# Kernel tuning notes

Measured on AMD Instinct MI355X. Metric: run time of the kernel, lower is better.

## Reference

```python
import jax, jax.numpy as jnp
import numpy as np

GAMMA = 1.0
N, M, D = 8192, 8192, 256


def setup_inputs() -> dict:
    key = jax.random.key(0)
    kx, ky = jax.random.split(key)
    x = jax.random.normal(kx, (N, D), dtype=jnp.float32)
    y = jax.random.normal(ky, (M, D), dtype=jnp.float32)
    return {"x": x, "y": y}


def reference(x, y):
    # Pairwise squared distances without materializing the (n, m, d) diff
    x2 = jnp.sum(x * x, axis=-1)              # (n,)
    y2 = jnp.sum(y * y, axis=-1)              # (m,)
    xy = jnp.einsum('nd,md->nm', x, y)        # (n, m)
    dist_sq = x2[:, None] + y2[None, :] - 2.0 * xy
    # clamp tiny negative values from cancellation to preserve exp(-g*d2)<=1
    dist_sq = jnp.maximum(dist_sq, 0.0)
    return jnp.exp(-GAMMA * dist_sq)
```

## Files before the change

### kernel.cpp

```cpp
#include <hip/hip_runtime.h>
#include <hip/hip_bf16.h>

typedef __attribute__((ext_vector_type(4))) float f32x4;
typedef __attribute__((ext_vector_type(8))) short bf16x8;
typedef __attribute__((ext_vector_type(16))) float f32x16;
typedef long i64t;

#define MSZ 8192
#define D_DIM 256
#define BM 128
#define BN 128
#define NTILES 8

#define GLOAD_LDS(g, s) __builtin_amdgcn_global_load_lds( \
    (const __attribute__((address_space(1))) unsigned int*)(g), \
    (__attribute__((address_space(3))) unsigned int*)(s), 16, 0, 0)

__device__ __forceinline__ unsigned short f2bf(float f) {
  __hip_bfloat16 h = __float2bfloat16(f);
  unsigned short u; __builtin_memcpy(&u, &h, 2); return u;
}

__global__ __launch_bounds__(256)
void prep_fp8(const float* __restrict__ X, const float* __restrict__ Y,
              unsigned char* __restrict__ Xq, unsigned char* __restrict__ Yq,
              float* __restrict__ x2, float* __restrict__ y2) {
  int gw = (blockIdx.x * 256 + threadIdx.x) >> 6;
  int l = threadIdx.x & 63;
  int row = gw & (MSZ - 1);
  const float* src = (gw < MSZ ? X : Y) + (size_t)row * D_DIM + l * 4;
  f32x4 v = *(const f32x4*)src;
  float ss = v[0]*v[0] + v[1]*v[1] + v[2]*v[2] + v[3]*v[3];
  int p = __builtin_amdgcn_cvt_pk_fp8_f32(v[0], v[1], 0, false);
  p = __builtin_amdgcn_cvt_pk_fp8_f32(v[2], v[3], p, true);
  unsigned char* dst = (gw < MSZ ? Xq : Yq) + (size_t)row * D_DIM + l * 4;
  *(unsigned int*)dst = (unsigned int)p;
  #pragma unroll
  for (int m = 1; m < 64; m <<= 1) ss += __shfl_xor(ss, m);
  if (l == 0) (gw < MSZ ? x2 : y2)[row] = ss;
}

__global__ __launch_bounds__(256, 2)
void rbf_main(const unsigned char* __restrict__ Xq, const unsigned char* __restrict__ Yq,
              const float* __restrict__ X2, const float* __restrict__ Y2,
              float* __restrict__ Out) {
  __shared__ __align__(16) unsigned char Al[BM * D_DIM];
  __shared__ __align__(16) unsigned char Bl[BN * D_DIM];
  __shared__ float sx2[BM];

  int bid = blockIdx.x;
  int swz = (bid & 7) * 64 + (bid >> 3);
  int bm = swz >> 3;
  int rowBase = bm * BM;
  int colBase = ((swz & 7) << 3) * BN;

  int tid = threadIdx.x;
  int l = tid & 63;
  int w = tid >> 6;
  int wr = w >> 1, wc = w & 1;

  if (tid < BM) sx2[tid] = X2[rowBase + tid];

  #pragma unroll
  for (int q = 0; q < 8; ++q) {
    int c = tid + 256 * q;
    int row = c >> 4, g = c & 15;
    GLOAD_LDS(Xq + (size_t)(rowBase + row) * D_DIM + (((g ^ (row & 15))) << 4), Al + c * 16);
  }
  float cy0 = Y2[colBase + wc * 64 + (l & 31)];
  float cy1 = Y2[colBase + wc * 64 + 32 + (l & 31)];
  #pragma unroll
  for (int q = 0; q < 8; ++q) {
    int c = tid + 256 * q;
    int row = c >> 4, g = c & 15;
    GLOAD_LDS(Yq + (size_t)(colBase + row) * D_DIM + (((g ^ (row & 15))) << 4), Bl + c * 16);
  }
  asm volatile("s_waitcnt lgkmcnt(0)" ::: "memory");

  const unsigned char* Abase = Al + (wr * 64 + (l & 31)) * D_DIM + ((l >> 5) << 3);
  const unsigned char* Bbase = Bl + (wc * 64 + (l & 31)) * D_DIM + ((l >> 5) << 3);
  int sk = l & 15;
  int h4 = (l >> 5) * 4;
  int kq = (l & 31) >> 2;

  #pragma unroll 1
  for (int tt = 0; tt < NTILES; ++tt) {
    if (tt == 0) asm volatile("s_waitcnt vmcnt(0)" ::: "memory");
    else         asm volatile("s_waitcnt vmcnt(16)" ::: "memory");
    __builtin_amdgcn_s_barrier();

    float sy0 = cy0, sy1 = cy1;
    int colC = colBase;

    f32x16 acc[2][2] = {};
    #pragma unroll
    for (int kk = 0; kk < 16; ++kk) {
      int ca = (kk ^ sk) << 4;
      i64t a0 = *(const i64t*)(Abase + ca);
      i64t a1 = *(const i64t*)(Abase + 32 * D_DIM + ca);
      i64t b0 = *(const i64t*)(Bbase + ca);
      i64t b1 = *(const i64t*)(Bbase + 32 * D_DIM + ca);
      acc[0][0] = __builtin_amdgcn_mfma_f32_32x32x16_fp8_fp8(a0, b0, acc[0][0], 0, 0, 0);
      acc[0][1] = __builtin_amdgcn_mfma_f32_32x32x16_fp8_fp8(a0, b1, acc[0][1], 0, 0, 0);
      acc[1][0] = __builtin_amdgcn_mfma_f32_32x32x16_fp8_fp8(a1, b0, acc[1][0], 0, 0, 0);
      acc[1][1] = __builtin_amdgcn_mfma_f32_32x32x16_fp8_fp8(a1, b1, acc[1][1], 0, 0, 0);
    }
    __builtin_amdgcn_s_barrier();

    if (tt + 1 < NTILES) {
      colBase += BN;
      cy0 = Y2[colBase + wc * 64 + (l & 31)];
      cy1 = Y2[colBase + wc * 64 + 32 + (l & 31)];
      #pragma unroll
      for (int q = 0; q < 8; ++q) {
        int c = tid + 256 * q;
        int row = c >> 4, g = c & 15;
        GLOAD_LDS(Yq + (size_t)(colBase + row) * D_DIM + (((g ^ (row & 15))) << 4), Bl + c * 16);
      }
    }
    asm volatile("" ::: "memory");

    #pragma unroll
    for (int i = 0; i < 2; ++i) {
      #pragma unroll
      for (int j = 0; j < 2; ++j) {
        float sy = j ? sy1 : sy0;
        #pragma unroll
        for (int g = 0; g < 4; ++g) {
          int rb0 = wr * 64 + i * 32 + g * 8 + h4;
          float p0, p1, p2, p3;
          {
            float sxa = sx2[rb0 + 0], sxb = sx2[rb0 + 1];
            float sxc = sx2[rb0 + 2], sxd = sx2[rb0 + 3];
            p0 = __expf(-fmaxf(fmaf(-2.0f, acc[i][j][g * 4 + 0], sxa + sy), 0.0f));
            p1 = __expf(-fmaxf(fmaf(-2.0f, acc[i][j][g * 4 + 1], sxb + sy), 0.0f));
            p2 = __expf(-fmaxf(fmaf(-2.0f, acc[i][j][g * 4 + 2], sxc + sy), 0.0f));
            p3 = __expf(-fmaxf(fmaf(-2.0f, acc[i][j][g * 4 + 3], sxd + sy), 0.0f));
          }
          {
            float s01 = (l & 1) ? p0 : p1;
            float r01 = __shfl_xor(s01, 1);
            if (l & 1) p0 = r01; else p1 = r01;
            float s23 = (l & 1) ? p2 : p3;
            float r23 = __shfl_xor(s23, 1);
            if (l & 1) p2 = r23; else p3 = r23;
            float s02 = (l & 2) ? p0 : p2;
            float r02 = __shfl_xor(s02, 2);
            if (l & 2) p0 = r02; else p2 = r02;
            float s13 = (l & 2) ? p1 : p3;
            float r13 = __shfl_xor(s13, 2);
            if (l & 2) p1 = r13; else p3 = r13;
          }
          int rowS = rowBase + rb0 + (l & 3);
          int colS = colC + wc * 64 + j * 32 + kq * 4;
          f32x4 v; v[0] = p0; v[1] = p1; v[2] = p2; v[3] = p3;
          *(f32x4*)(Out + (size_t)rowS * MSZ + colS) = v;
        }
      }
    }
  }
}

__global__ __launch_bounds__(256, 2)
void rbf_mfma_kernel(const float* __restrict__ X, const float* __restrict__ Y,
                     float* __restrict__ Out) {
  __shared__ unsigned short As[BM * 64];
  __shared__ unsigned short Bs[BN * 64];
  __shared__ float sx2[BM];
  __shared__ float sy2[BN];
  int bid = blockIdx.x;
  int cpx = gridDim.x >> 3;
  int swz = (bid & 7) * cpx + (bid >> 3);
  int bm = swz >> 6, bn = swz & 63;
  int rowBase = bm * BM, colBase = bn * BN;
  int tid = threadIdx.x;
  int l = tid & 63;
  int w = tid >> 6;
  int wr = w >> 1, wc = w & 1;
  f32x4 acc[4][4] = {};
  float assq[4] = {0.f,0.f,0.f,0.f};
  float bssq[4] = {0.f,0.f,0.f,0.f};
  for (int ks = 0; ks < D_DIM / 64; ++ks) {
    if (ks) __syncthreads();
    #pragma unroll
    for (int p = 0; p < 4; ++p) {
      int c = tid + 256 * p;
      int r = c >> 3;
      int kc = c & 7;
      const float* gx = X + (size_t)(rowBase + r) * D_DIM + ks * 64 + kc * 8;
      const float* gy = Y + (size_t)(colBase + r) * D_DIM + ks * 64 + kc * 8;
      f32x4 xa = *(const f32x4*)gx;
      f32x4 xb = *(const f32x4*)(gx + 4);
      f32x4 ya = *(const f32x4*)gy;
      f32x4 yb = *(const f32x4*)(gy + 4);
      #pragma unroll
      for (int j = 0; j < 4; ++j) {
        assq[p] += xa[j]*xa[j] + xb[j]*xb[j];
        bssq[p] += ya[j]*ya[j] + yb[j]*yb[j];
      }
      union { bf16x8 v; unsigned short u[8]; } pa, pb;
      #pragma unroll
      for (int j = 0; j < 4; ++j) {
        pa.u[j] = f2bf(xa[j]);  pa.u[j+4] = f2bf(xb[j]);
        pb.u[j] = f2bf(ya[j]);  pb.u[j+4] = f2bf(yb[j]);
      }
      int boff = (r * 128 + kc * 16) ^ ((r & 7) << 4);
      *(bf16x8*)((char*)As + boff) = pa.v;
      *(bf16x8*)((char*)Bs + boff) = pb.v;
    }
    __syncthreads();
    #pragma unroll
    for (int kk = 0; kk < 2; ++kk) {
      bf16x8 af[4], bfv[4];
      #pragma unroll
      for (int i = 0; i < 4; ++i) {
        int ra = wr*64 + i*16 + (l & 15);
        int offa = (ra * 128 + kk*64 + (l >> 4) * 16) ^ ((ra & 7) << 4);
        af[i] = *(bf16x8*)((char*)As + offa);
        int rb = wc*64 + i*16 + (l & 15);
        int offb = (rb * 128 + kk*64 + (l >> 4) * 16) ^ ((rb & 7) << 4);
        bfv[i] = *(bf16x8*)((char*)Bs + offb);
      }
      #pragma unroll
      for (int i = 0; i < 4; ++i)
        #pragma unroll
        for (int j = 0; j < 4; ++j)
          acc[i][j] = __builtin_amdgcn_mfma_f32_16x16x32_bf16(af[i], bfv[j], acc[i][j], 0, 0, 0);
    }
  }
  #pragma unroll
  for (int p = 0; p < 4; ++p) {
    float a = assq[p], b = bssq[p];
    a += __shfl_xor(a, 1); b += __shfl_xor(b, 1);
    a += __shfl_xor(a, 2); b += __shfl_xor(b, 2);
    a += __shfl_xor(a, 4); b += __shfl_xor(b, 4);
    if ((tid & 7) == 0) {
      int r = (tid >> 3) + 32 * p;
      sx2[r] = a;
      sy2[r] = b;
    }
  }
  __syncthreads();
  #pragma unroll
  for (int i = 0; i < 4; ++i)
    #pragma unroll
    for (int j = 0; j < 4; ++j)
      #pragma unroll
      for (int q = 0; q < 4; ++q) {
        int rn = wr*64 + i*16 + (l >> 4) * 4 + q;
        int cm = wc*64 + j*16 + (l & 15);
        float d2 = sx2[rn] + sy2[cm] - 2.0f * acc[i][j][q];
        Out[(size_t)(rowBase + rn) * MSZ + (colBase + cm)] = __expf(-fmaxf(d2, 0.0f));
      }
}

extern "C" void kernel_launch(void* const* d_in, const int* in_sizes, int n_in,
                              void* d_out, int out_size, void* d_ws, size_t ws_size,
                              hipStream_t stream) {
  const float* X = (const float*)d_in[0];
  const float* Y = (const float*)d_in[1];
  float* Out = (float*)d_out;
  const size_t QB = (size_t)MSZ * D_DIM;
  const size_t NEED = QB * 2 + (size_t)MSZ * 4 * 2;
  if (ws_size >= NEED) {
    unsigned char* Xq = (unsigned char*)d_ws;
    unsigned char* Yq = Xq + QB;
    float* x2 = (float*)(Yq + QB);
    float* y2 = x2 + MSZ;
    prep_fp8<<<dim3(4096), dim3(256), 0, stream>>>(X, Y, Xq, Yq, x2, y2);
    rbf_main<<<dim3(512), dim3(256), 0, stream>>>(Xq, Yq, x2, y2, Out);
  } else {
    rbf_mfma_kernel<<<dim3(64 * 64), dim3(256), 0, stream>>>(X, Y, Out);
  }
}
```

Before: 69.41 us.

## Keep A fragments in registers, double-buffer B tiles, and use nontemporal scalar stores

Loads the X tile once into LDS, moves the A fragments and row norms into registers, then reuses LDS as a double buffer for Y tiles. The next tile is prefetched while the current one is computed, which is meant to hide global-load latency and remove the second barrier per tile. The epilogue drops the shuffle transpose and writes each element with a scalar nontemporal store. That adds VGPR pressure from about 32 i64 fragments plus 32 floats, and replaces 16-byte stores with 4-byte stores.

After: 86.23 us. 24.2% more time.

```diff
diff --git a/kernel.cpp b/kernel.cpp
--- a/kernel.cpp
+++ b/kernel.cpp
@@ -44,8 +44,7 @@
 void rbf_main(const unsigned char* __restrict__ Xq, const unsigned char* __restrict__ Yq,
               const float* __restrict__ X2, const float* __restrict__ Y2,
               float* __restrict__ Out) {
-  __shared__ __align__(16) unsigned char Al[BM * D_DIM];
-  __shared__ __align__(16) unsigned char Bl[BN * D_DIM];
+  __shared__ __align__(16) unsigned char Bl[2][32768];
   __shared__ float sx2[BM];
 
   int bid = blockIdx.x;
@@ -58,6 +57,7 @@
   int l = tid & 63;
   int w = tid >> 6;
   int wr = w >> 1, wc = w & 1;
+  int sk = l & 15;
 
   if (tid < BM) sx2[tid] = X2[rowBase + tid];
 
@@ -65,99 +65,97 @@
   for (int q = 0; q < 8; ++q) {
     int c = tid + 256 * q;
     int row = c >> 4, g = c & 15;
-    GLOAD_LDS(Xq + (size_t)(rowBase + row) * D_DIM + (((g ^ (row & 15))) << 4), Al + c * 16);
-  }
+    GLOAD_LDS(Xq + (size_t)(rowBase + row) * D_DIM + ((g ^ (row & 15)) << 4),
+              (unsigned char*)Bl[0] + c * 16);
+  }
+  asm volatile("s_waitcnt vmcnt(0)" ::: "memory");
+  __syncthreads();
+
+  const unsigned char* Ab = (const unsigned char*)Bl[0] + (wr * 64 + (l & 31)) * D_DIM + ((l >> 5) << 3);
+  i64t afr[2][16];
+  #pragma unroll
+  for (int i = 0; i < 2; ++i)
+    #pragma unroll
+    for (int kk = 0; kk < 16; ++kk)
+      afr[i][kk] = *(const i64t*)(Ab + i * 32 * D_DIM + ((kk ^ sk) << 4));
+  float sxv[2][16];
+  int rbq = wr * 64 + 4 * (l >> 5);
+  #pragma unroll
+  for (int i = 0; i < 2; ++i)
+    #pragma unroll
+    for (int q = 0; q < 16; ++q)
+      sxv[i][q] = sx2[rbq + i * 32 + (q & 3) + 8 * (q >> 2)];
+  __syncthreads();
+
   float cy0 = Y2[colBase + wc * 64 + (l & 31)];
   float cy1 = Y2[colBase + wc * 64 + 32 + (l & 31)];
   #pragma unroll
   for (int q = 0; q < 8; ++q) {
     int c = tid + 256 * q;
     int row = c >> 4, g = c & 15;
-    GLOAD_LDS(Yq + (size_t)(colBase + row) * D_DIM + (((g ^ (row & 15))) << 4), Bl + c * 16);
-  }
-  asm volatile("s_waitcnt lgkmcnt(0)" ::: "memory");
-
-  const unsigned char* Abase = Al + (wr * 64 + (l & 31)) * D_DIM + ((l >> 5) << 3);
-  const unsigned char* Bbase = Bl + (wc * 64 + (l & 31)) * D_DIM + ((l >> 5) << 3);
-  int sk = l & 15;
-  int h4 = (l >> 5) * 4;
-  int kq = (l & 31) >> 2;
+    GLOAD_LDS(Yq + (size_t)(colBase + row) * D_DIM + ((g ^ (row & 15)) << 4),
+              (unsigned char*)Bl[0] + c * 16);
+  }
 
   #pragma unroll 1
   for (int tt = 0; tt < NTILES; ++tt) {
-    if (tt == 0) asm volatile("s_waitcnt vmcnt(0)" ::: "memory");
-    else         asm volatile("s_waitcnt vmcnt(16)" ::: "memory");
+    int colC = colBase + tt * BN;
+    float sy0 = cy0, sy1 = cy1;
+
     __builtin_amdgcn_s_barrier();
-
-    float sy0 = cy0, sy1 = cy1;
-    int colC = colBase;
-
-    f32x16 acc[2][2] = {};
-    #pragma unroll
-    for (int kk = 0; kk < 16; ++kk) {
-      int ca = (kk ^ sk) << 4;
-      i64t a0 = *(const i64t*)(Abase + ca);
-      i64t a1 = *(const i64t*)(Abase + 32 * D_DIM + ca);
-      i64t b0 = *(const i64t*)(Bbase + ca);
-      i64t b1 = *(const i64t*)(Bbase + 32 * D_DIM + ca);
-      acc[0][0] = __builtin_amdgcn_mfma_f32_32x32x16_fp8_fp8(a0, b0, acc[0][0], 0, 0, 0);
-      acc[0][1] = __builtin_amdgcn_mfma_f32_32x32x16_fp8_fp8(a0, b1, acc[0][1], 0, 0, 0);
-      acc[1][0] = __builtin_amdgcn_mfma_f32_32x32x16_fp8_fp8(a1, b0, acc[1][0], 0, 0, 0);
-      acc[1][1] = __builtin_amdgcn_mfma_f32_32x32x16_fp8_fp8(a1, b1, acc[1][1], 0, 0, 0);
-    }
-    __builtin_amdgcn_s_barrier();
+    asm volatile("" ::: "memory");
 
     if (tt + 1 < NTILES) {
-      colBase += BN;
-      cy0 = Y2[colBase + wc * 64 + (l & 31)];
-      cy1 = Y2[colBase + wc * 64 + 32 + (l & 31)];
+      int colN = colBase + (tt + 1) * BN;
+      cy0 = Y2[colN + wc * 64 + (l & 31)];
+      cy1 = Y2[colN + wc * 64 + 32 + (l & 31)];
+      unsigned char* dst = (unsigned char*)Bl[(tt + 1) & 1];
       #pragma unroll
       for (int q = 0; q < 8; ++q) {
         int c = tid + 256 * q;
         int row = c >> 4, g = c & 15;
-        GLOAD_LDS(Yq + (size_t)(colBase + row) * D_DIM + (((g ^ (row & 15))) << 4), Bl + c * 16);
-      }
-    }
+        GLOAD_LDS(Yq + (size_t)(colN + row) * D_DIM + ((g ^ (row & 15)) << 4), dst + c * 16);
+      }
+    }
+    asm volatile("" ::: "memory");
+
+    if (tt == 0)          asm volatile("s_waitcnt vmcnt(10)" ::: "memory");
+    if (tt == NTILES - 1) asm volatile("s_waitcnt vmcnt(48)" ::: "memory");
+    __builtin_amdgcn_s_barrier();
+    __builtin_amdgcn_sched_barrier(0);
+
+    const unsigned char* Bb = (const unsigned char*)Bl[tt & 1] + (wc * 64 + (l & 31)) * D_DIM + ((l >> 5) << 3);
+    f32x16 acc[2][2] = {};
+    #pragma unroll
+    for (int kk = 0; kk < 16; ++kk) {
+      int ca = (kk ^ sk) << 4;
+      i64t b0 = *(const i64t*)(Bb + ca);
+      i64t b1 = *(const i64t*)(Bb + 32 * D_DIM + ca);
+      acc[0][0] = __builtin_amdgcn_mfma_f32_32x32x16_fp8_fp8(afr[0][kk], b0, acc[0][0], 0, 0, 0);
+      acc[0][1] = __builtin_amdgcn_mfma_f32_32x32x16_fp8_fp8(afr[0][kk], b1, acc[0][1], 0, 0, 0);
+      acc[1][0] = __builtin_amdgcn_mfma_f32_32x32x16_fp8_fp8(afr[1][kk], b0, acc[1][0], 0, 0, 0);
+      acc[1][1] = __builtin_amdgcn_mfma_f32_32x32x16_fp8_fp8(afr[1][kk], b1, acc[1][1], 0, 0, 0);
+    }
+    __builtin_amdgcn_sched_barrier(0);
     asm volatile("" ::: "memory");
 
     #pragma unroll
     for (int i = 0; i < 2; ++i) {
+      int rb0 = wr * 64 + i * 32 + 4 * (l >> 5);
+      float* base = Out + (size_t)(rowBase + rb0) * MSZ + colC + wc * 64 + (l & 31);
       #pragma unroll
       for (int j = 0; j < 2; ++j) {
         float sy = j ? sy1 : sy0;
         #pragma unroll
-        for (int g = 0; g < 4; ++g) {
-          int rb0 = wr * 64 + i * 32 + g * 8 + h4;
-          float p0, p1, p2, p3;
-          {
-            float sxa = sx2[rb0 + 0], sxb = sx2[rb0 + 1];
-            float sxc = sx2[rb0 + 2], sxd = sx2[rb0 + 3];
-            p0 = __expf(-fmaxf(fmaf(-2.0f, acc[i][j][g * 4 + 0], sxa + sy), 0.0f));
-            p1 = __expf(-fmaxf(fmaf(-2.0f, acc[i][j][g * 4 + 1], sxb + sy), 0.0f));
-            p2 = __expf(-fmaxf(fmaf(-2.0f, acc[i][j][g * 4 + 2], sxc + sy), 0.0f));
-            p3 = __expf(-fmaxf(fmaf(-2.0f, acc[i][j][g * 4 + 3], sxd + sy), 0.0f));
-          }
-          {
-            float s01 = (l & 1) ? p0 : p1;
-            float r01 = __shfl_xor(s01, 1);
-            if (l & 1) p0 = r01; else p1 = r01;
-            float s23 = (l & 1) ? p2 : p3;
-            float r23 = __shfl_xor(s23, 1);
-            if (l & 1) p2 = r23; else p3 = r23;
-            float s02 = (l & 2) ? p0 : p2;
-            float r02 = __shfl_xor(s02, 2);
-            if (l & 2) p0 = r02; else p2 = r02;
-            float s13 = (l & 2) ? p1 : p3;
-            float r13 = __shfl_xor(s13, 2);
-            if (l & 2) p1 = r13; else p3 = r13;
-          }
-          int rowS = rowBase + rb0 + (l & 3);
-          int colS = colC + wc * 64 + j * 32 + kq * 4;
-          f32x4 v; v[0] = p0; v[1] = p1; v[2] = p2; v[3] = p3;
-          *(f32x4*)(Out + (size_t)rowS * MSZ + colS) = v;
+        for (int q = 0; q < 16; ++q) {
+          int rpat = (q & 3) + 8 * (q >> 2);
+          float d = fmaf(-2.0f, acc[i][j][q], sxv[i][q] + sy);
+          __builtin_nontemporal_store(__expf(-fmaxf(d, 0.0f)),
+                                      base + (size_t)rpat * MSZ + j * 32);
         }
       }
     }
+    asm volatile("" ::: "memory");
   }
 }
 
```

## Store RBF outputs as scalar coalesced rows instead of shuffled float4 stores

Applied to the files above, without the earlier changes.

The epilogue drops the lane-shuffle transpose that built float4 stores. Each lane now writes its accumulator elements directly as scalar stores, with 32 lanes covering contiguous columns. All Y2 norms for the block's tiles are preloaded into LDS up front, and the vmcnt wait threshold is relaxed from 16 to 63 so more stores can stay in flight while the next B tile loads. A sched_barrier is added as well. The change removes shuffle/select work and per-tile global Y2 loads, but issues four times as many store instructions, each 128B-coalesced per half-wave.

Measured after the change: 61.56 us. -11.3%, faster.

```diff
diff --git a/kernel.cpp b/kernel.cpp
--- a/kernel.cpp
+++ b/kernel.cpp
@@ -47,6 +47,7 @@
   __shared__ __align__(16) unsigned char Al[BM * D_DIM];
   __shared__ __align__(16) unsigned char Bl[BN * D_DIM];
   __shared__ float sx2[BM];
+  __shared__ float sy2l[NTILES * BN];
 
   int bid = blockIdx.x;
   int swz = (bid & 7) * 64 + (bid >> 3);
@@ -58,39 +59,34 @@
   int l = tid & 63;
   int w = tid >> 6;
   int wr = w >> 1, wc = w & 1;
+  int sk = l & 15;
 
   if (tid < BM) sx2[tid] = X2[rowBase + tid];
+  *(f32x4*)&sy2l[tid * 4] = *(const f32x4*)&Y2[colBase + tid * 4];
 
   #pragma unroll
   for (int q = 0; q < 8; ++q) {
     int c = tid + 256 * q;
     int row = c >> 4, g = c & 15;
-    GLOAD_LDS(Xq + (size_t)(rowBase + row) * D_DIM + (((g ^ (row & 15))) << 4), Al + c * 16);
-  }
-  float cy0 = Y2[colBase + wc * 64 + (l & 31)];
-  float cy1 = Y2[colBase + wc * 64 + 32 + (l & 31)];
+    GLOAD_LDS(Xq + (size_t)(rowBase + row) * D_DIM + ((g ^ (row & 15)) << 4), Al + c * 16);
+  }
   #pragma unroll
   for (int q = 0; q < 8; ++q) {
     int c = tid + 256 * q;
     int row = c >> 4, g = c & 15;
-    GLOAD_LDS(Yq + (size_t)(colBase + row) * D_DIM + (((g ^ (row & 15))) << 4), Bl + c * 16);
+    GLOAD_LDS(Yq + (size_t)(colBase + row) * D_DIM + ((g ^ (row & 15)) << 4), Bl + c * 16);
   }
   asm volatile("s_waitcnt lgkmcnt(0)" ::: "memory");
 
   const unsigned char* Abase = Al + (wr * 64 + (l & 31)) * D_DIM + ((l >> 5) << 3);
   const unsigned char* Bbase = Bl + (wc * 64 + (l & 31)) * D_DIM + ((l >> 5) << 3);
-  int sk = l & 15;
-  int h4 = (l >> 5) * 4;
-  int kq = (l & 31) >> 2;
 
   #pragma unroll 1
   for (int tt = 0; tt < NTILES; ++tt) {
     if (tt == 0) asm volatile("s_waitcnt vmcnt(0)" ::: "memory");
-    else         asm volatile("s_waitcnt vmcnt(16)" ::: "memory");
+    else         asm volatile("s_waitcnt vmcnt(63)" ::: "memory");
     __builtin_amdgcn_s_barrier();
-
-    float sy0 = cy0, sy1 = cy1;
-    int colC = colBase;
+    __builtin_amdgcn_sched_barrier(0);
 
     f32x16 acc[2][2] = {};
     #pragma unroll
@@ -106,58 +102,37 @@
       acc[1][1] = __builtin_amdgcn_mfma_f32_32x32x16_fp8_fp8(a1, b1, acc[1][1], 0, 0, 0);
     }
     __builtin_amdgcn_s_barrier();
+    asm volatile("" ::: "memory");
 
     if (tt + 1 < NTILES) {
-      colBase += BN;
-      cy0 = Y2[colBase + wc * 64 + (l & 31)];
-      cy1 = Y2[colBase + wc * 64 + 32 + (l & 31)];
+      int colN = colBase + (tt + 1) * BN;
       #pragma unroll
       for (int q = 0; q < 8; ++q) {
         int c = tid + 256 * q;
         int row = c >> 4, g = c & 15;
-        GLOAD_LDS(Yq + (size_t)(colBase + row) * D_DIM + (((g ^ (row & 15))) << 4), Bl + c * 16);
+        GLOAD_LDS(Yq + (size_t)(colN + row) * D_DIM + ((g ^ (row & 15)) << 4), Bl + c * 16);
       }
     }
     asm volatile("" ::: "memory");
 
+    float sy0 = sy2l[tt * BN + wc * 64 + (l & 31)];
+    float sy1 = sy2l[tt * BN + wc * 64 + 32 + (l & 31)];
     #pragma unroll
     for (int i = 0; i < 2; ++i) {
+      int rb0 = wr * 64 + i * 32 + 4 * (l >> 5);
+      float* base = Out + (size_t)(rowBase + rb0) * MSZ + colBase + tt * BN + wc * 64 + (l & 31);
       #pragma unroll
       for (int j = 0; j < 2; ++j) {
         float sy = j ? sy1 : sy0;
         #pragma unroll
-        for (int g = 0; g < 4; ++g) {
-          int rb0 = wr * 64 + i * 32 + g * 8 + h4;
-          float p0, p1, p2, p3;
-          {
-            float sxa = sx2[rb0 + 0], sxb = sx2[rb0 + 1];
-            float sxc = sx2[rb0 + 2], sxd = sx2[rb0 + 3];
-            p0 = __expf(-fmaxf(fmaf(-2.0f, acc[i][j][g * 4 + 0], sxa + sy), 0.0f));
-            p1 = __expf(-fmaxf(fmaf(-2.0f, acc[i][j][g * 4 + 1], sxb + sy), 0.0f));
-            p2 = __expf(-fmaxf(fmaf(-2.0f, acc[i][j][g * 4 + 2], sxc + sy), 0.0f));
-            p3 = __expf(-fmaxf(fmaf(-2.0f, acc[i][j][g * 4 + 3], sxd + sy), 0.0f));
-          }
-          {
-            float s01 = (l & 1) ? p0 : p1;
-            float r01 = __shfl_xor(s01, 1);
-            if (l & 1) p0 = r01; else p1 = r01;
-            float s23 = (l & 1) ? p2 : p3;
-            float r23 = __shfl_xor(s23, 1);
-            if (l & 1) p2 = r23; else p3 = r23;
-            float s02 = (l & 2) ? p0 : p2;
-            float r02 = __shfl_xor(s02, 2);
-            if (l & 2) p0 = r02; else p2 = r02;
-            float s13 = (l & 2) ? p1 : p3;
-            float r13 = __shfl_xor(s13, 2);
-            if (l & 2) p1 = r13; else p3 = r13;
-          }
-          int rowS = rowBase + rb0 + (l & 3);
-          int colS = colC + wc * 64 + j * 32 + kq * 4;
-          f32x4 v; v[0] = p0; v[1] = p1; v[2] = p2; v[3] = p3;
-          *(f32x4*)(Out + (size_t)rowS * MSZ + colS) = v;
+        for (int q = 0; q < 16; ++q) {
+          int rpat = (q & 3) + 8 * (q >> 2);
+          float d = fmaf(-2.0f, acc[i][j][q], sx2[rb0 + rpat] + sy);
+          base[(size_t)rpat * MSZ + j * 32] = __expf(-fmaxf(d, 0.0f));
         }
       }
     }
+    asm volatile("" ::: "memory");
   }
 }
 
```
